# Optimization experiments

Measured on AMD Instinct MI355X. Metric: run time of the kernel, lower is better.

The kernel has to match this reference:

```python
import jax, jax.numpy as jnp
import numpy as np

N = 50000      # nodes
C = 16         # input features
NT = 4         # diffusion scales
K1 = 4         # anisotropic kernels
KEIG = 128     # Laplacian eigenpairs
E = 1600000    # edges
HID = 512
OUT = 256


def setup_inputs() -> dict:
    key = jax.random.key(0)
    ks = jax.random.split(key, 10)
    x = jax.random.normal(ks[0], (N, C), dtype=jnp.float32)
    evals = jax.random.uniform(ks[1], (KEIG,), dtype=jnp.float32)
    evecs = jax.random.normal(ks[2], (N, KEIG), dtype=jnp.float32)
    taus = jax.random.uniform(ks[3], (NT,), dtype=jnp.float32)
    kvals = jax.random.normal(ks[4], (K1, E), dtype=jnp.float32)
    edge_index = jax.random.randint(ks[5], (2, E), 0, N, dtype=jnp.int64)
    W1 = jax.random.normal(ks[6], (C * NT * K1, HID), dtype=jnp.float32) * 0.05
    b1 = jnp.zeros((HID,), dtype=jnp.float32)
    W2 = jax.random.normal(ks[7], (HID, OUT), dtype=jnp.float32) * 0.05
    b2 = jnp.zeros((OUT,), dtype=jnp.float32)
    return {"x": x, "evals": evals, "evecs": evecs, "taus": taus,
            "kvals": kvals, "edge_index": edge_index,
            "W1": W1, "b1": b1, "W2": W2, "b2": b2}


def _diffusion(x, evals, evecs, taus):
    # Spectral heat diffusion at NT learned scales, concatenated on channels.
    coeff = evecs.T @ x                                   # [KEIG, C]
    scales = jnp.exp(-evals[None, :] * taus[:, None])      # [NT, KEIG]
    # [N, NT, C] = evecs @ (scale_t * coeff) per scale
    diff = jnp.einsum('nk,tk,kc->ntc', evecs, scales, coeff)
    return diff.reshape(x.shape[0], -1)                    # [N, NT*C]


def _aniso_conv(x, edge_index, kvals):
    # out_k[i] = sum_{edges j->i} K_k[edge] * x[j]; concat over kernels.
    src, dst = edge_index[0], edge_index[1]
    n = x.shape[0]
    outs = []
    for k in range(kvals.shape[0]):  # small fixed loop over K1 kernels
        msgs = kvals[k][:, None] * x[src]                  # [E, NT*C]
        outs.append(jax.ops.segment_sum(msgs, dst, num_segments=n))
    return jnp.concatenate(outs, axis=-1)                  # [N, K1*NT*C]


def reference(x, evals, evecs, taus, kvals, edge_index, W1, b1, W2, b2):
    h = _diffusion(x, evals, evecs, taus)                  # [N, NT*C]
    h = _aniso_conv(h, edge_index, kvals)                  # [N, K1*NT*C]
    h = jax.nn.relu(h @ W1 + b1)                           # MLP layer 1
    h = h @ W2 + b2                                        # MLP layer 2
    # L2 normalize per node (F.normalize with eps=1e-12)
    nrm = jnp.maximum(jnp.linalg.norm(h, axis=-1, keepdims=True), 1e-12)
    return h / nrm
```

## Files before the change

kernel.cpp:

```cpp
#include <hip/hip_runtime.h>

typedef __bf16 bf16_t;
typedef __attribute__((ext_vector_type(8))) __bf16 bf16x8;
typedef __attribute__((ext_vector_type(4))) float f32x4;
typedef unsigned int uint;
typedef unsigned short ushort;

#define N_NODES 50000
#define C_IN 16
#define NT 4
#define K1 4
#define KEIG 128
#define E_EDGES 1600000
#define HID 512
#define OUT_F 256
#define FEAT 64
#define CONVF 256
#define M_PAD 50048
#define CPB 1024
#define RED1 64
#define NB 782
#define CAP_B 2432
#define BSB 391
#define EPT 16

__device__ inline uint bfbits(float f) {
    bf16_t b = (bf16_t)f;
    return (uint)__builtin_bit_cast(unsigned short, b);
}
__device__ inline float bfu(uint u) {
    return __uint_as_float(u << 16);
}

__global__ void coeff_partial_kernel(const float* __restrict__ evecs,
                                     const float* __restrict__ x,
                                     float* __restrict__ partial,
                                     bf16_t* __restrict__ evb, int n) {
    __shared__ float lds[4 * 2048];
    int t = threadIdx.x, lane = t & 63, wid = t >> 6;
    int gw = blockIdx.x * 4 + wid;
    int total_w = gridDim.x * 4;
    int rpw = (n + total_w - 1) / total_w;
    int r0 = gw * rpw;
    int r1 = min(n, r0 + rpw);
    float acc0[16], acc1[16];
#pragma unroll
    for (int c = 0; c < 16; c++) { acc0[c] = 0.f; acc1[c] = 0.f; }
    for (int r = r0; r < r1; r++) {
        float e0 = evecs[(size_t)r * KEIG + lane];
        float e1 = evecs[(size_t)r * KEIG + 64 + lane];
        evb[(size_t)r * KEIG + lane] = (bf16_t)e0;
        evb[(size_t)r * KEIG + 64 + lane] = (bf16_t)e1;
        const float* xr = &x[(size_t)r * C_IN];
#pragma unroll
        for (int c = 0; c < 16; c++) {
            float xv = xr[c];
            acc0[c] += e0 * xv;
            acc1[c] += e1 * xv;
        }
    }
#pragma unroll
    for (int c = 0; c < 16; c++) {
        lds[wid * 2048 + c * 128 + lane] = acc0[c];
        lds[wid * 2048 + c * 128 + 64 + lane] = acc1[c];
    }
    __syncthreads();
    for (int idx = t; idx < 2048; idx += 256) {
        float s = lds[idx] + lds[2048 + idx] + lds[4096 + idx] + lds[6144 + idx];
        partial[(size_t)blockIdx.x * 2048 + idx] = s;
    }
}

__global__ void coeff_reduce1_kernel(const float* __restrict__ partial,
                                     float* __restrict__ partial2) {
    int g = blockIdx.x >> 3;
    int idx = (blockIdx.x & 7) * 256 + threadIdx.x;
    float s = 0.f;
#pragma unroll
    for (int j = 0; j < 16; j++)
        s += partial[(size_t)(g * 16 + j) * 2048 + idx];
    partial2[(size_t)g * 2048 + idx] = s;
}

__global__ void coeff_reduce2_kernel(const float* __restrict__ partial2,
                                     float* __restrict__ coeff) {
    int idx = blockIdx.x * 256 + threadIdx.x;
    float s = 0.f;
#pragma unroll 8
    for (int b = 0; b < RED1; b++) s += partial2[(size_t)b * 2048 + idx];
    coeff[idx] = s;
}

__global__ void sc2t_kernel(const float* __restrict__ evals,
                            const float* __restrict__ taus,
                            const float* __restrict__ coeff,
                            bf16_t* __restrict__ sc2t) {
    int idx = blockIdx.x * 256 + threadIdx.x;
    int col = idx >> 7, k = idx & 127;
    float v = expf(-evals[k] * taus[col >> 4]) * coeff[(col & 15) * 128 + k];
    sc2t[col * KEIG + k] = (bf16_t)v;
}

#define DSTR 136
__global__ void diffusion_mfma_kernel(const bf16_t* __restrict__ evb,
                                      const bf16_t* __restrict__ sc2t,
                                      bf16_t* __restrict__ diffb) {
    __shared__ bf16_t Alds[128 * DSTR];
    __shared__ bf16_t Blds[64 * DSTR];
    const int t = threadIdx.x;
    const int lane = t & 63;
    const int wid = t >> 6;
    const int row0 = blockIdx.x * 128;
#pragma unroll
    for (int i = 0; i < 8; i++) {
        int idx = t + i * 256;
        int r = idx >> 4;
        int k8 = (idx & 15) * 8;
        *(uint4*)&Alds[r * DSTR + k8] =
            *(const uint4*)&evb[(size_t)(row0 + r) * KEIG + k8];
    }
#pragma unroll
    for (int i = 0; i < 4; i++) {
        int idx = t + i * 256;
        int r = idx >> 4;
        int k8 = (idx & 15) * 8;
        *(uint4*)&Blds[r * DSTR + k8] =
            *(const uint4*)&sc2t[r * KEIG + k8];
    }
    __syncthreads();
    f32x4 acc[2][4];
#pragma unroll
    for (int m = 0; m < 2; m++)
#pragma unroll
        for (int n = 0; n < 4; n++) acc[m][n] = (f32x4){0.f, 0.f, 0.f, 0.f};
#pragma unroll
    for (int kk = 0; kk < 128; kk += 32) {
        int ko = kk + ((lane >> 4) << 3);
        bf16x8 av[2], bv[4];
#pragma unroll
        for (int m = 0; m < 2; m++)
            av[m] = *(const bf16x8*)&Alds[(wid * 32 + m * 16 + (lane & 15)) * DSTR + ko];
#pragma unroll
        for (int n = 0; n < 4; n++)
            bv[n] = *(const bf16x8*)&Blds[(n * 16 + (lane & 15)) * DSTR + ko];
#pragma unroll
        for (int m = 0; m < 2; m++)
#pragma unroll
            for (int n = 0; n < 4; n++)
                acc[m][n] = __builtin_amdgcn_mfma_f32_16x16x32_bf16(
                    av[m], bv[n], acc[m][n], 0, 0, 0);
    }
#pragma unroll
    for (int m = 0; m < 2; m++) {
#pragma unroll
        for (int n = 0; n < 4; n++) {
            int col = n * 16 + (lane & 15);
#pragma unroll
            for (int q = 0; q < 4; q++) {
                int row = row0 + wid * 32 + m * 16 + ((lane >> 4) << 2) + q;
                diffb[(size_t)row * FEAT + col] = (bf16_t)acc[m][n][q];
            }
        }
    }
}

__global__ void binscatter_kernel(const int* __restrict__ src,
                                  const int* __restrict__ dst,
                                  const float* __restrict__ kvals,
                                  int* __restrict__ cursor,
                                  int4* __restrict__ bucket, int E) {
    __shared__ int lcnt[NB];
    __shared__ int lbase[NB];
    int t = threadIdx.x;
    for (int i = t; i < NB; i += 256) lcnt[i] = 0;
    __syncthreads();
    int e0 = blockIdx.x * (EPT * 256);
    int d[EPT];
#pragma unroll
    for (int i = 0; i < EPT; i++) {
        int e = e0 + i * 256 + t;
        d[i] = (e < E) ? dst[e] : -1;
        if (d[i] >= 0) atomicAdd(&lcnt[d[i] >> 6], 1);
    }
    __syncthreads();
    for (int i = t; i < NB; i += 256) {
        int c = lcnt[i];
        lbase[i] = c ? atomicAdd(&cursor[i * 16], c) : 0;
    }
    __syncthreads();
    for (int i = t; i < NB; i += 256) lcnt[i] = 0;
    __syncthreads();
#pragma unroll
    for (int i = 0; i < EPT; i++) {
        if (d[i] < 0) continue;
        int e = e0 + i * 256 + t;
        int b = d[i] >> 6;
        int r = atomicAdd(&lcnt[b], 1);
        int slot = lbase[b] + r;
        uint w01 = bfbits(kvals[e]) | (bfbits(kvals[(size_t)E + e]) << 16);
        uint w23 = bfbits(kvals[2 * (size_t)E + e]) | (bfbits(kvals[3 * (size_t)E + e]) << 16);
        int4 rec;
        rec.x = src[e]; rec.y = (int)w01; rec.z = (int)w23; rec.w = d[i] & 63;
        if (slot < CAP_B) bucket[(size_t)b * CAP_B + slot] = rec;
    }
}

__global__ void bucket_scan_kernel(const int* __restrict__ cursor,
                                   int* __restrict__ bucket_base,
                                   int* __restrict__ row_start) {
    __shared__ int lds[1024];
    int t = threadIdx.x;
    int own = (t < NB) ? cursor[t * 16] : 0;
    lds[t] = own;
    __syncthreads();
    for (int off = 1; off < 1024; off <<= 1) {
        int v = (t >= off) ? lds[t - off] : 0;
        __syncthreads();
        lds[t] += v;
        __syncthreads();
    }
    if (t < NB) bucket_base[t] = lds[t] - own;
    if (t == 0) row_start[N_NODES] = E_EDGES;
}

__global__ void localsort_kernel(const int4* __restrict__ bucket,
                                 const int* __restrict__ cursor,
                                 const int* __restrict__ bucket_base,
                                 int4* __restrict__ csr_rec,
                                 int* __restrict__ row_start) {
    __shared__ int cnt[64];
    __shared__ int off[64];
    int b = blockIdx.x, t = threadIdx.x;
    int n = cursor[b * 16];
    if (n > CAP_B) n = CAP_B;
    int base = bucket_base[b];
    if (t < 64) cnt[t] = 0;
    __syncthreads();
    for (int i = t; i < n; i += 256)
        atomicAdd(&cnt[bucket[(size_t)b * CAP_B + i].w], 1);
    __syncthreads();
    if (t == 0) {
        int run = 0;
#pragma unroll
        for (int j = 0; j < 64; j++) { off[j] = run; run += cnt[j]; }
    }
    __syncthreads();
    if (t < 64) {
        int g = b * 64 + t;
        if (g < N_NODES) row_start[g] = base + off[t];
        cnt[t] = 0;
    }
    __syncthreads();
    for (int i = t; i < n; i += 256) {
        int4 rec = bucket[(size_t)b * CAP_B + i];
        int r = atomicAdd(&cnt[rec.w], 1);
        csr_rec[(size_t)(base + off[rec.w] + r)] = rec;
    }
}

__global__ void aniso_kernel(const bf16_t* __restrict__ diffb_,
                             const int* __restrict__ row_start,
                             const int4* __restrict__ csr_rec,
                             bf16_t* __restrict__ conv, int n) {
    const ushort* diffb = (const ushort*)diffb_;
    int wid = (blockIdx.x * 256 + threadIdx.x) >> 6;
    int lane = threadIdx.x & 63;
    if (wid >= n) return;
    int start = __builtin_amdgcn_readfirstlane(row_start[wid]);
    int end = __builtin_amdgcn_readfirstlane(row_start[wid + 1]);
    float a0 = 0.f, a1 = 0.f, a2 = 0.f, a3 = 0.f;
    int p = start;
    for (; p + 8 <= end; p += 8) {
        int s[8];
        uint wy[8], wz[8];
#pragma unroll
        for (int j = 0; j < 8; j++) {
            int4 rec = csr_rec[p + j];
            s[j] = rec.x; wy[j] = (uint)rec.y; wz[j] = (uint)rec.z;
        }
        float h[8];
#pragma unroll
        for (int j = 0; j < 8; j++)
            h[j] = bfu((uint)diffb[(size_t)s[j] * FEAT + lane]);
#pragma unroll
        for (int j = 0; j < 8; j++) {
            a0 += __uint_as_float(wy[j] << 16) * h[j];
            a1 += __uint_as_float(wy[j] & 0xffff0000u) * h[j];
            a2 += __uint_as_float(wz[j] << 16) * h[j];
            a3 += __uint_as_float(wz[j] & 0xffff0000u) * h[j];
        }
    }
    for (; p < end; p++) {
        int4 rec = csr_rec[p];
        float h0 = bfu((uint)diffb[(size_t)rec.x * FEAT + lane]);
        uint y = (uint)rec.y, z = (uint)rec.z;
        a0 += __uint_as_float(y << 16) * h0;
        a1 += __uint_as_float(y & 0xffff0000u) * h0;
        a2 += __uint_as_float(z << 16) * h0;
        a3 += __uint_as_float(z & 0xffff0000u) * h0;
    }
    size_t base = (size_t)wid * CONVF + lane;
    conv[base]       = (bf16_t)a0;
    conv[base + 64]  = (bf16_t)a1;
    conv[base + 128] = (bf16_t)a2;
    conv[base + 192] = (bf16_t)a3;
}

__global__ void convw_kernel(const float* __restrict__ W, bf16_t* __restrict__ Wt,
                             int rows, int cols) {
    int idx = blockIdx.x * 256 + threadIdx.x;
    if (idx >= rows * cols) return;
    int o = idx / rows, f = idx % rows;
    Wt[idx] = (bf16_t)W[(size_t)f * cols + o];
}

#define BM 128
#define BN 128
#define BK 64
#define LSTR 72

template <int EPI>
__global__ void gemm_bf16_kernel(const bf16_t* __restrict__ A,
                                 const bf16_t* __restrict__ Bt,
                                 const float* __restrict__ bias,
                                 void* __restrict__ Cout,
                                 int Nn, int K, int Mvalid) {
    __shared__ bf16_t Alds[BM * LSTR];
    __shared__ bf16_t Blds[BN * LSTR];
    const int t = threadIdx.x;
    const int lane = t & 63;
    const int wid = t >> 6;
    const int row0 = blockIdx.y * BM;
    const int col0 = blockIdx.x * BN;
    const int wr = (wid >> 1) * 64;
    const int wc = (wid & 1) * 64;

    f32x4 acc[4][4];
#pragma unroll
    for (int m = 0; m < 4; m++)
#pragma unroll
        for (int n = 0; n < 4; n++) acc[m][n] = (f32x4){0.f, 0.f, 0.f, 0.f};

    for (int kt = 0; kt < K; kt += BK) {
#pragma unroll
        for (int i = 0; i < 4; i++) {
            int idx = t + i * 256;
            int r = idx >> 3;
            int k8 = (idx & 7) * 8;
            *(uint4*)&Alds[r * LSTR + k8] =
                *(const uint4*)&A[(size_t)(row0 + r) * K + kt + k8];
            *(uint4*)&Blds[r * LSTR + k8] =
                *(const uint4*)&Bt[(size_t)(col0 + r) * K + kt + k8];
        }
        __syncthreads();
#pragma unroll
        for (int kk = 0; kk < BK; kk += 32) {
            int ko = kk + ((lane >> 4) << 3);
            bf16x8 av[4], bv[4];
#pragma unroll
            for (int m = 0; m < 4; m++)
                av[m] = *(const bf16x8*)&Alds[(wr + m * 16 + (lane & 15)) * LSTR + ko];
#pragma unroll
            for (int n = 0; n < 4; n++)
                bv[n] = *(const bf16x8*)&Blds[(wc + n * 16 + (lane & 15)) * LSTR + ko];
#pragma unroll
            for (int m = 0; m < 4; m++)
#pragma unroll
                for (int n = 0; n < 4; n++)
                    acc[m][n] = __builtin_amdgcn_mfma_f32_16x16x32_bf16(
                        av[m], bv[n], acc[m][n], 0, 0, 0);
        }
        __syncthreads();
    }

#pragma unroll
    for (int n = 0; n < 4; n++) {
        int col = col0 + wc + n * 16 + (lane & 15);
        float bvl = bias[col];
#pragma unroll
        for (int m = 0; m < 4; m++) {
#pragma unroll
            for (int r = 0; r < 4; r++) {
                int row = row0 + wr + m * 16 + ((lane >> 4) << 2) + r;
                float v = acc[m][n][r] + bvl;
                if (EPI == 0) {
                    v = v > 0.f ? v : 0.f;
                    ((bf16_t*)Cout)[(size_t)row * Nn + col] = (bf16_t)v;
                } else {
                    if (row < Mvalid)
                        ((float*)Cout)[(size_t)row * Nn + col] = v;
                }
            }
        }
    }
}

__global__ void norm_kernel(float* __restrict__ out, int n) {
    int w = (blockIdx.x * 256 + threadIdx.x) >> 6;
    int lane = threadIdx.x & 63;
    if (w >= n) return;
    float4 v = *(float4*)&out[(size_t)w * OUT_F + lane * 4];
    float ss = v.x * v.x + v.y * v.y + v.z * v.z + v.w * v.w;
#pragma unroll
    for (int off = 32; off > 0; off >>= 1) ss += __shfl_xor(ss, off);
    float nrm = sqrtf(ss);
    nrm = nrm > 1e-12f ? nrm : 1e-12f;
    float sc = 1.f / nrm;
    v.x *= sc; v.y *= sc; v.z *= sc; v.w *= sc;
    *(float4*)&out[(size_t)w * OUT_F + lane * 4] = v;
}

extern "C" void kernel_launch(void* const* d_in, const int* in_sizes, int n_in,
                              void* d_out, int out_size, void* d_ws, size_t ws_size,
                              hipStream_t stream) {
    const float* x      = (const float*)d_in[0];
    const float* evals  = (const float*)d_in[1];
    const float* evecs  = (const float*)d_in[2];
    const float* taus   = (const float*)d_in[3];
    const float* kvals  = (const float*)d_in[4];
    const int*   eidx   = (const int*)d_in[5];
    const float* W1     = (const float*)d_in[6];
    const float* b1     = (const float*)d_in[7];
    const float* W2     = (const float*)d_in[8];
    const float* b2     = (const float*)d_in[9];
    float* out = (float*)d_out;

    const int N = N_NODES, E = E_EDGES;
    const int* e_src = eidx;
    const int* e_dst = eidx + E;

    char* ws = (char*)d_ws;
    size_t off = 0;
    auto alloc = [&](size_t bytes) {
        void* p = ws + off;
        off = (off + bytes + 255) & ~(size_t)255;
        return p;
    };
    float* coeff       = (float*)alloc(2048 * 4);
    float* partial     = (float*)alloc((size_t)CPB * 2048 * 4);
    float* partial2    = (float*)alloc((size_t)RED1 * 2048 * 4);
    bf16_t* evb        = (bf16_t*)alloc((size_t)M_PAD * KEIG * 2);
    bf16_t* sc2t       = (bf16_t*)alloc((size_t)FEAT * KEIG * 2);
    bf16_t* diffb      = (bf16_t*)alloc((size_t)M_PAD * FEAT * 2);
    int*   cursor      = (int*)alloc((size_t)NB * 16 * 4);
    int*   bucket_base = (int*)alloc((size_t)(NB + 1) * 4);
    int*   row_start   = (int*)alloc((size_t)(N + 1) * 4);
    size_t csr_bytes = (size_t)E * 16;
    size_t h1_bytes  = (size_t)M_PAD * HID * 2;
    int4*  csr_rec   = (int4*)alloc(csr_bytes > h1_bytes ? csr_bytes : h1_bytes);
    bf16_t* h1       = (bf16_t*)csr_rec;
    size_t bucket_bytes = (size_t)NB * CAP_B * 16;
    size_t conv_bytes   = (size_t)M_PAD * CONVF * 2;
    int4*  bucket    = (int4*)alloc(bucket_bytes > conv_bytes ? bucket_bytes : conv_bytes);
    bf16_t* conv     = (bf16_t*)bucket;
    bf16_t* w1t      = (bf16_t*)alloc((size_t)HID * CONVF * 2);
    bf16_t* w2t      = (bf16_t*)alloc((size_t)OUT_F * HID * 2);
    (void)ws_size;

    hipMemsetAsync(cursor, 0, (size_t)NB * 16 * 4, stream);

    coeff_partial_kernel<<<CPB, 256, 0, stream>>>(evecs, x, partial, evb, N);
    coeff_reduce1_kernel<<<RED1 * 8, 256, 0, stream>>>(partial, partial2);
    coeff_reduce2_kernel<<<8, 256, 0, stream>>>(partial2, coeff);
    sc2t_kernel<<<32, 256, 0, stream>>>(evals, taus, coeff, sc2t);
    diffusion_mfma_kernel<<<M_PAD / 128, 256, 0, stream>>>(evb, sc2t, diffb);

    binscatter_kernel<<<BSB, 256, 0, stream>>>(e_src, e_dst, kvals, cursor, bucket, E);
    bucket_scan_kernel<<<1, 1024, 0, stream>>>(cursor, bucket_base, row_start);
    localsort_kernel<<<NB, 256, 0, stream>>>(bucket, cursor, bucket_base,
                                             csr_rec, row_start);

    aniso_kernel<<<(N + 3) / 4, 256, 0, stream>>>(diffb, row_start, csr_rec, conv, N);

    convw_kernel<<<(CONVF * HID + 255) / 256, 256, 0, stream>>>(W1, w1t, CONVF, HID);
    convw_kernel<<<(HID * OUT_F + 255) / 256, 256, 0, stream>>>(W2, w2t, HID, OUT_F);

    dim3 g1(HID / BN, M_PAD / BM);
    gemm_bf16_kernel<0><<<g1, 256, 0, stream>>>(conv, w1t, b1, h1, HID, CONVF, N);
    dim3 g2(OUT_F / BN, M_PAD / BM);
    gemm_bf16_kernel<1><<<g2, 256, 0, stream>>>(h1, w2t, b2, out, OUT_F, HID, N);

    norm_kernel<<<(N + 3) / 4, 256, 0, stream>>>(out, N);
}
```

Measured before the change: 221.3 us.

## Restructure edge bucketing into LDS-staged two-pass radix sort with coarser buckets

Replaces the 782-bucket global scatter with a radix pass that first sorts each block's 2048 edges by coarse bucket (256 nodes) in LDS, then writes contiguous runs to 196 global buckets. The second pass sorts each coarse bucket by its 256 local destinations into CSR. The aim is more coalesced global writes and fewer global atomics in the scatter. In exchange it costs extra LDS staging and larger per-bucket sort work with only 196 blocks in the second pass, which may underfill the GPU.

```diff
diff --git a/kernel.cpp b/kernel.cpp
--- a/kernel.cpp
+++ b/kernel.cpp
@@ -5,6 +5,7 @@
 typedef __attribute__((ext_vector_type(4))) float f32x4;
 typedef unsigned int uint;
 typedef unsigned short ushort;
+typedef unsigned char uchar;
 
 #define N_NODES 50000
 #define C_IN 16
@@ -19,10 +20,10 @@
 #define M_PAD 50048
 #define CPB 1024
 #define RED1 64
-#define NB 782
-#define CAP_B 2432
-#define BSB 391
-#define EPT 16
+#define SH_C 8
+#define NBC 196
+#define CAPC 8704
+#define PA_B 782
 
 __device__ inline uint bfbits(float f) {
     bf16_t b = (bf16_t)f;
@@ -164,97 +165,123 @@
     }
 }
 
-__global__ void binscatter_kernel(const int* __restrict__ src,
-                                  const int* __restrict__ dst,
-                                  const float* __restrict__ kvals,
-                                  int* __restrict__ cursor,
-                                  int4* __restrict__ bucket, int E) {
-    __shared__ int lcnt[NB];
-    __shared__ int lbase[NB];
+__global__ void radixA_kernel(const int* __restrict__ src,
+                              const int* __restrict__ dst,
+                              const float* __restrict__ kvals,
+                              int* __restrict__ gcursor,
+                              int4* __restrict__ bucket, int E) {
+    __shared__ int hist[256];
+    __shared__ int lds_off[256];
+    __shared__ int cnt2[256];
+    __shared__ int run_base[256];
+    __shared__ int4 recs[2048];
+    __shared__ uchar posb[2048];
     int t = threadIdx.x;
-    for (int i = t; i < NB; i += 256) lcnt[i] = 0;
-    __syncthreads();
-    int e0 = blockIdx.x * (EPT * 256);
-    int d[EPT];
-#pragma unroll
-    for (int i = 0; i < EPT; i++) {
-        int e = e0 + i * 256 + t;
-        d[i] = (e < E) ? dst[e] : -1;
-        if (d[i] >= 0) atomicAdd(&lcnt[d[i] >> 6], 1);
-    }
-    __syncthreads();
-    for (int i = t; i < NB; i += 256) {
-        int c = lcnt[i];
-        lbase[i] = c ? atomicAdd(&cursor[i * 16], c) : 0;
-    }
-    __syncthreads();
-    for (int i = t; i < NB; i += 256) lcnt[i] = 0;
-    __syncthreads();
-#pragma unroll
-    for (int i = 0; i < EPT; i++) {
-        if (d[i] < 0) continue;
-        int e = e0 + i * 256 + t;
-        int b = d[i] >> 6;
-        int r = atomicAdd(&lcnt[b], 1);
-        int slot = lbase[b] + r;
+    hist[t] = 0; cnt2[t] = 0;
+    __syncthreads();
+    int e0 = blockIdx.x * 2048;
+    int total = min(2048, E - e0);
+    int d[8];
+#pragma unroll
+    for (int j = 0; j < 8; j++) {
+        int e = e0 + j * 256 + t;
+        d[j] = (e < E) ? dst[e] : -1;
+        if (d[j] >= 0) atomicAdd(&hist[d[j] >> SH_C], 1);
+    }
+    __syncthreads();
+    int own = hist[t];
+    lds_off[t] = own;
+    __syncthreads();
+    for (int o = 1; o < 256; o <<= 1) {
+        int v = (t >= o) ? lds_off[t - o] : 0;
+        __syncthreads();
+        lds_off[t] += v;
+        __syncthreads();
+    }
+    int excl = lds_off[t] - own;
+    __syncthreads();
+    lds_off[t] = excl;
+    __syncthreads();
+#pragma unroll
+    for (int j = 0; j < 8; j++) {
+        if (d[j] < 0) continue;
+        int e = e0 + j * 256 + t;
+        int b = d[j] >> SH_C;
+        int r = atomicAdd(&cnt2[b], 1);
+        int pos = lds_off[b] + r;
         uint w01 = bfbits(kvals[e]) | (bfbits(kvals[(size_t)E + e]) << 16);
         uint w23 = bfbits(kvals[2 * (size_t)E + e]) | (bfbits(kvals[3 * (size_t)E + e]) << 16);
         int4 rec;
-        rec.x = src[e]; rec.y = (int)w01; rec.z = (int)w23; rec.w = d[i] & 63;
-        if (slot < CAP_B) bucket[(size_t)b * CAP_B + slot] = rec;
-    }
-}
-
-__global__ void bucket_scan_kernel(const int* __restrict__ cursor,
-                                   int* __restrict__ bucket_base,
+        rec.x = src[e]; rec.y = (int)w01; rec.z = (int)w23; rec.w = d[j] & 255;
+        recs[pos] = rec;
+        posb[pos] = (uchar)b;
+    }
+    if (t < NBC) {
+        int c = hist[t];
+        run_base[t] = c ? atomicAdd(&gcursor[t * 16], c) : 0;
+    }
+    __syncthreads();
+    for (int i = t; i < total; i += 256) {
+        int b = posb[i];
+        int g = run_base[b] + (i - lds_off[b]);
+        if (g < CAPC) bucket[(size_t)b * CAPC + g] = recs[i];
+    }
+}
+
+__global__ void coarse_scan_kernel(const int* __restrict__ gcursor,
+                                   int* __restrict__ coarse_base,
                                    int* __restrict__ row_start) {
-    __shared__ int lds[1024];
+    __shared__ int lds[256];
     int t = threadIdx.x;
-    int own = (t < NB) ? cursor[t * 16] : 0;
+    int own = (t < NBC) ? min(gcursor[t * 16], CAPC) : 0;
     lds[t] = own;
     __syncthreads();
-    for (int off = 1; off < 1024; off <<= 1) {
-        int v = (t >= off) ? lds[t - off] : 0;
+    for (int o = 1; o < 256; o <<= 1) {
+        int v = (t >= o) ? lds[t - o] : 0;
         __syncthreads();
         lds[t] += v;
         __syncthreads();
     }
-    if (t < NB) bucket_base[t] = lds[t] - own;
-    if (t == 0) row_start[N_NODES] = E_EDGES;
-}
-
-__global__ void localsort_kernel(const int4* __restrict__ bucket,
-                                 const int* __restrict__ cursor,
-                                 const int* __restrict__ bucket_base,
-                                 int4* __restrict__ csr_rec,
-                                 int* __restrict__ row_start) {
-    __shared__ int cnt[64];
-    __shared__ int off[64];
+    if (t < NBC) coarse_base[t] = lds[t] - own;
+    if (t == 255) row_start[N_NODES] = lds[255];
+}
+
+__global__ void radixB_kernel(const int4* __restrict__ bucket,
+                              const int* __restrict__ gcursor,
+                              const int* __restrict__ coarse_base,
+                              int4* __restrict__ csr_rec,
+                              int* __restrict__ row_start) {
+    __shared__ int hist[256];
+    __shared__ int off[256];
+    __shared__ int cnt2[256];
     int b = blockIdx.x, t = threadIdx.x;
-    int n = cursor[b * 16];
-    if (n > CAP_B) n = CAP_B;
-    int base = bucket_base[b];
-    if (t < 64) cnt[t] = 0;
-    __syncthreads();
-    for (int i = t; i < n; i += 256)
-        atomicAdd(&cnt[bucket[(size_t)b * CAP_B + i].w], 1);
-    __syncthreads();
-    if (t == 0) {
-        int run = 0;
-#pragma unroll
-        for (int j = 0; j < 64; j++) { off[j] = run; run += cnt[j]; }
-    }
-    __syncthreads();
-    if (t < 64) {
-        int g = b * 64 + t;
-        if (g < N_NODES) row_start[g] = base + off[t];
-        cnt[t] = 0;
-    }
-    __syncthreads();
+    int n = min(gcursor[b * 16], CAPC);
+    int base = coarse_base[b];
+    hist[t] = 0; cnt2[t] = 0;
+    __syncthreads();
+    const int4* brec = &bucket[(size_t)b * CAPC];
+    for (int i = t; i < n; i += 256) atomicAdd(&hist[brec[i].w & 255], 1);
+    __syncthreads();
+    int own = hist[t];
+    off[t] = own;
+    __syncthreads();
+    for (int o = 1; o < 256; o <<= 1) {
+        int v = (t >= o) ? off[t - o] : 0;
+        __syncthreads();
+        off[t] += v;
+        __syncthreads();
+    }
+    int excl = off[t] - own;
+    __syncthreads();
+    off[t] = excl;
+    __syncthreads();
+    int g = b * 256 + t;
+    if (g < N_NODES) row_start[g] = base + off[t];
     for (int i = t; i < n; i += 256) {
-        int4 rec = bucket[(size_t)b * CAP_B + i];
-        int r = atomicAdd(&cnt[rec.w], 1);
-        csr_rec[(size_t)(base + off[rec.w] + r)] = rec;
+        int4 rec = brec[i];
+        int w = rec.w & 255;
+        int r = atomicAdd(&cnt2[w], 1);
+        csr_rec[(size_t)(base + off[w] + r)] = rec;
     }
 }
 
@@ -442,14 +469,14 @@
     bf16_t* evb        = (bf16_t*)alloc((size_t)M_PAD * KEIG * 2);
     bf16_t* sc2t       = (bf16_t*)alloc((size_t)FEAT * KEIG * 2);
     bf16_t* diffb      = (bf16_t*)alloc((size_t)M_PAD * FEAT * 2);
-    int*   cursor      = (int*)alloc((size_t)NB * 16 * 4);
-    int*   bucket_base = (int*)alloc((size_t)(NB + 1) * 4);
+    int*   gcursor     = (int*)alloc((size_t)NBC * 16 * 4);
+    int*   coarse_base = (int*)alloc((size_t)(NBC + 1) * 4);
     int*   row_start   = (int*)alloc((size_t)(N + 1) * 4);
     size_t csr_bytes = (size_t)E * 16;
     size_t h1_bytes  = (size_t)M_PAD * HID * 2;
     int4*  csr_rec   = (int4*)alloc(csr_bytes > h1_bytes ? csr_bytes : h1_bytes);
     bf16_t* h1       = (bf16_t*)csr_rec;
-    size_t bucket_bytes = (size_t)NB * CAP_B * 16;
+    size_t bucket_bytes = (size_t)NBC * CAPC * 16;
     size_t conv_bytes   = (size_t)M_PAD * CONVF * 2;
     int4*  bucket    = (int4*)alloc(bucket_bytes > conv_bytes ? bucket_bytes : conv_bytes);
     bf16_t* conv     = (bf16_t*)bucket;
@@ -457,7 +484,7 @@
     bf16_t* w2t      = (bf16_t*)alloc((size_t)OUT_F * HID * 2);
     (void)ws_size;
 
-    hipMemsetAsync(cursor, 0, (size_t)NB * 16 * 4, stream);
+    hipMemsetAsync(gcursor, 0, (size_t)NBC * 16 * 4, stream);
 
     coeff_partial_kernel<<<CPB, 256, 0, stream>>>(evecs, x, partial, evb, N);
     coeff_reduce1_kernel<<<RED1 * 8, 256, 0, stream>>>(partial, partial2);
@@ -465,10 +492,10 @@
     sc2t_kernel<<<32, 256, 0, stream>>>(evals, taus, coeff, sc2t);
     diffusion_mfma_kernel<<<M_PAD / 128, 256, 0, stream>>>(evb, sc2t, diffb);
 
-    binscatter_kernel<<<BSB, 256, 0, stream>>>(e_src, e_dst, kvals, cursor, bucket, E);
-    bucket_scan_kernel<<<1, 1024, 0, stream>>>(cursor, bucket_base, row_start);
-    localsort_kernel<<<NB, 256, 0, stream>>>(bucket, cursor, bucket_base,
-                                             csr_rec, row_start);
+    radixA_kernel<<<PA_B, 256, 0, stream>>>(e_src, e_dst, kvals, gcursor, bucket, E);
+    coarse_scan_kernel<<<1, 256, 0, stream>>>(gcursor, coarse_base, row_start);
+    radixB_kernel<<<NBC, 256, 0, stream>>>(bucket, gcursor, coarse_base,
+                                           csr_rec, row_start);
 
     aniso_kernel<<<(N + 3) / 4, 256, 0, stream>>>(diffb, row_start, csr_rec, conv, N);
 
```

Result: no change. 219.8 us (-0.7%).
